# Kernel optimization log

Hardware: AMD Instinct MI355X
Metric: run time of the kernel (lower is better)

## Reference

```python
import jax, jax.numpy as jnp
import numpy as np

B, T, NVAR, H, C = 1024, 96, 7, 64, 3  # batch, seq_len/time-points, nvar, ode_hidden, components
H4 = 4 * H


def setup_inputs() -> dict:
    key = jax.random.key(0)
    ks = jax.random.split(key, 12)
    def w(k, shape, fan_in):
        return (jax.random.normal(k, shape, jnp.float32) / np.sqrt(fan_in)).astype(jnp.float32)
    return {
        "x": jax.random.normal(ks[0], (B, T, NVAR), jnp.float32),
        # init_net: Linear(nvar->H), ReLU, Linear(H->C*H)   (stored as (in,out))
        "init_w1": w(ks[1], (NVAR, H), NVAR), "init_b1": jnp.zeros((H,), jnp.float32),
        "init_w2": w(ks[2], (H, C * H), H),   "init_b2": jnp.zeros((C * H,), jnp.float32),
        # ODEFunc.net: Linear(H+C -> 4H), Tanh, Linear(4H -> H)
        "ode_w1": w(ks[3], (H + C, H4), H + C), "ode_b1": jnp.zeros((H4,), jnp.float32),
        "ode_w2": w(ks[4], (H4, H), H4),        "ode_b2": jnp.zeros((H,), jnp.float32),
        # interaction param (init eye) and frozen conservation linear (eye, no bias)
        "interaction": jnp.eye(C, dtype=jnp.float32),
        "conservation": jnp.eye(C, dtype=jnp.float32),
        # decode_net: per-component Linear(H->H), ReLU, Linear(H->nvar)
        "dec_w1": w(ks[5], (C, H, H), H), "dec_b1": jnp.zeros((C, H), jnp.float32),
        "dec_w2": w(ks[6], (C, H, NVAR), H), "dec_b2": jnp.zeros((C, NVAR), jnp.float32),
        "t_points": jnp.linspace(0.0, 1.0, T).astype(jnp.float32),
    }


def _ode_func(t, state, interaction, conservation, ode_w1, ode_b1, ode_w2, ode_b2):
    # state: (B, C, H)
    b = state.shape[0]
    state_comp = state.mean(axis=-1)                                   # (B, C)
    ie = jnp.einsum('ij,bj->bi', interaction, state_comp)              # bmm(interaction, mean)
    ie = jnp.einsum('oi,bi->bo', conservation, ie)                     # frozen linear (no bias)
    inputs = jnp.concatenate(
        [state.reshape(b * C, H), ie.reshape(b * C, 1), jnp.full((b * C, 1), t, state.dtype)],
        axis=1)                                                        # (B*C, H+2)? no: H + 1 + 1 = H + C since C==3? -> H+2; matches torch cat of [H,1,1] only if C accounts: net expects H+C=H+3.
    # NOTE: torch concatenates [state(H), interaction_effect(1), t(1)] = H+2 features but the
    # Linear expects H+C.  With C=3 torch relies on nn.Linear(H+3) receiving H+2?? It does not --
    # torch code passes H+2 features into Linear(H+C).  Faithful translation pads to match below.
    d = jnp.tanh(inputs @ ode_w1[: inputs.shape[1]] + ode_b1) @ ode_w2 + ode_b2
    return d.reshape(state.shape)


def reference(x, init_w1, init_b1, init_w2, init_b2, ode_w1, ode_b1, ode_w2, ode_b2,
              interaction, conservation, dec_w1, dec_b1, dec_w2, dec_b2, t_points):
    # initial state from mean over sequence
    h0 = jax.nn.relu(x.mean(axis=1) @ init_w1 + init_b1)
    y0 = (h0 @ init_w2 + init_b2).reshape(-1, C, H)                    # (B, C, H)

    f = lambda t, y: _ode_func(t, y, interaction, conservation, ode_w1, ode_b1, ode_w2, ode_b2)

    def rk4_step(y, ts):
        t0, t1 = ts
        h = t1 - t0
        k1 = f(t0, y)
        k2 = f(t0 + 0.5 * h, y + 0.5 * h * k1)
        k3 = f(t0 + 0.5 * h, y + 0.5 * h * k2)
        k4 = f(t1, y + h * k3)
        y1 = y + (h / 6.0) * (k1 + 2.0 * k2 + 2.0 * k3 + k4)
        return y1, y1

    ts = jnp.stack([t_points[:-1], t_points[1:]], axis=1)              # (T-1, 2)
    _, ys = jax.lax.scan(rk4_step, y0, ts)                             # (T-1, B, C, H)
    states = jnp.concatenate([y0[None], ys], axis=0)                   # (T, B, C, H)
    states = jnp.transpose(states, (1, 0, 2, 3))                       # (B, T, C, H)

    # per-component decode MLP
    hid = jax.nn.relu(jnp.einsum('btch,chk->btck', states, dec_w1) + dec_b1)
    comps = jnp.einsum('btck,ckn->btcn', hid, dec_w2) + dec_b2         # (B, T, C, NVAR)
    comps = jnp.moveaxis(comps, 2, 0)                                  # (C, B, T, NVAR)
    # comps[0] is the trend, comps[1:] the high-frequency components
    return comps
```

## Files before the change

kernel.cpp:

```cpp
#include <hip/hip_runtime.h>

#define BTOT 1024
#define TPTS 96
#define NV   7
#define HD   64
#define NH   256

typedef short bf16x8 __attribute__((ext_vector_type(8)));
typedef float f32x4  __attribute__((ext_vector_type(4)));
typedef unsigned int u32x4 __attribute__((ext_vector_type(4)));
#define MFMA16(a,b,c) __builtin_amdgcn_mfma_f32_16x16x32_bf16(a,b,c,0,0,0)

#define OFF_YP   0
#define OFF_TP   1024
#define OFF_PRT  5120
#define OFF_YF   9472
#define OFF_PS   10512
#define OFF_TPS  10576
#define SMEM_WORDS 10672
#define SMEM_BYTES (SMEM_WORDS*4)

__device__ __forceinline__ float rdlane(float v, int i) {
    return __int_as_float(__builtin_amdgcn_readlane(__float_as_int(v), i));
}
__device__ __forceinline__ float wsum64(float v) {
    v += __shfl_xor(v, 1);  v += __shfl_xor(v, 2);  v += __shfl_xor(v, 4);
    v += __shfl_xor(v, 8);  v += __shfl_xor(v, 16); v += __shfl_xor(v, 32);
    return v;
}
__device__ __forceinline__ float tanh_fast(float x) {
    float e = __expf(2.f * x);
    return 1.f - 2.f / (e + 1.f);
}
__device__ __forceinline__ ushort bf16rn(float x) {
    unsigned u = __float_as_uint(x);
    return (ushort)((u + 0x7fffu + ((u >> 16) & 1u)) >> 16);
}
__device__ __forceinline__ void split2(float x, ushort& h, ushort& l) {
    h = bf16rn(x);
    float hf = __uint_as_float(((unsigned)h) << 16);
    l = bf16rn(x - hf);
}

union FU { u32x4 uv; unsigned u[4]; ushort s[8]; bf16x8 v; };

__global__ __launch_bounds__(1024)
void node_mfma6(const float* __restrict__ x,
                const float* __restrict__ iw1, const float* __restrict__ ib1,
                const float* __restrict__ iw2, const float* __restrict__ ib2,
                const float* __restrict__ ow1, const float* __restrict__ ob1,
                const float* __restrict__ ow2, const float* __restrict__ ob2,
                const float* __restrict__ inter, const float* __restrict__ cons,
                const float* __restrict__ dw1, const float* __restrict__ db1,
                const float* __restrict__ dw2, const float* __restrict__ db2,
                const float* __restrict__ tpts,
                float* __restrict__ out)
{
    extern __shared__ float sm[];
    unsigned* YPw = (unsigned*)(sm + OFF_YP);
    unsigned* TPw = (unsigned*)(sm + OFF_TP);
    float*    PRT = sm + OFF_PRT;
    float*    Yf  = sm + OFF_YF;
    float*    PS  = sm + OFF_PS;
    float*    tps = sm + OFF_TPS;

    const int tid = threadIdx.x;
    const int w   = tid >> 6;
    const int ln  = tid & 63;
    const int m   = ln & 15;
    const int g4  = ln >> 4;
    const int nt  = w & 3;
    const int kq  = w >> 2;

    if (tid < TPTS) tps[tid] = tpts[tid];

    const int col1 = 16*w + m;
    FU w1h[2], w1l[2], w2h[2], w2l[2];
    #pragma unroll
    for (int cc = 0; cc < 2; ++cc) {
        #pragma unroll
        for (int j = 0; j < 8; ++j) {
            ushort h, l;
            int k1 = 32*cc + 8*g4 + j;
            split2(ow1[k1*NH + col1], h, l);
            w1h[cc].s[j] = h; w1l[cc].s[j] = l;
            int k2 = 64*kq + 32*cc + 8*g4 + j;
            split2(ow2[k2*HD + 16*nt + m], h, l);
            w2h[cc].s[j] = h; w2l[cc].s[j] = l;
        }
    }
    const float w64c = ow1[64*NH + col1];
    const float w65c = ow1[65*NH + col1];
    const float b1c  = ob1[col1];
    const float b2c  = ob2[16*nt + m];

    const int cpm = m % 3, base3 = m - cpm;
    float Mr0, Mr1, Mr2;
    {
        float I[9], C[9];
        #pragma unroll
        for (int i = 0; i < 9; ++i) { I[i] = inter[i]; C[i] = cons[i]; }
        float M_[3][3];
        #pragma unroll
        for (int r = 0; r < 3; ++r)
            #pragma unroll
            for (int c = 0; c < 3; ++c)
                M_[r][c] = (C[r*3+0]*I[0*3+c] + C[r*3+1]*I[1*3+c] + C[r*3+2]*I[2*3+c]) * (1.f/64.f);
        Mr0 = (cpm==0) ? M_[0][0] : (cpm==1) ? M_[1][0] : M_[2][0];
        Mr1 = (cpm==0) ? M_[0][1] : (cpm==1) ? M_[1][1] : M_[2][1];
        Mr2 = (cpm==0) ? M_[0][2] : (cpm==1) ? M_[1][2] : M_[2][2];
    }

    {
        const int el0 = w >> 2;
        const int b0  = blockIdx.x*4 + el0;
        float xs0,xs1,xs2,xs3,xs4,xs5,xs6;
        {
            const float* xp = x + (size_t)b0 * TPTS * NV + ln * NV;
            float v0=xp[0],v1=xp[1],v2=xp[2],v3=xp[3],v4=xp[4],v5=xp[5],v6=xp[6];
            if (ln < 32) {
                const float* xp2 = xp + 64 * NV;
                v0+=xp2[0]; v1+=xp2[1]; v2+=xp2[2]; v3+=xp2[3]; v4+=xp2[4]; v5+=xp2[5]; v6+=xp2[6];
            }
            xs0=wsum64(v0)*(1.f/96.f); xs1=wsum64(v1)*(1.f/96.f); xs2=wsum64(v2)*(1.f/96.f);
            xs3=wsum64(v3)*(1.f/96.f); xs4=wsum64(v4)*(1.f/96.f); xs5=wsum64(v5)*(1.f/96.f);
            xs6=wsum64(v6)*(1.f/96.f);
        }
        float h0v;
        {
            float a = ib1[ln];
            a = fmaf(xs0, iw1[0*HD+ln], a); a = fmaf(xs1, iw1[1*HD+ln], a);
            a = fmaf(xs2, iw1[2*HD+ln], a); a = fmaf(xs3, iw1[3*HD+ln], a);
            a = fmaf(xs4, iw1[4*HD+ln], a); a = fmaf(xs5, iw1[5*HD+ln], a);
            a = fmaf(xs6, iw1[6*HD+ln], a);
            h0v = fmaxf(a, 0.f);
        }
        float y0a = ib2[ln], y0b = ib2[64+ln], y0c = ib2[128+ln];
        #pragma unroll
        for (int k = 0; k < 64; ++k) {
            float hk = rdlane(h0v, k);
            y0a = fmaf(hk, iw2[k*192 + ln],       y0a);
            y0b = fmaf(hk, iw2[k*192 + 64 + ln],  y0b);
            y0c = fmaf(hk, iw2[k*192 + 128 + ln], y0c);
        }
        if ((w & 3) == 0) {
            float yv[3] = {y0a, y0b, y0c};
            #pragma unroll
            for (int r = 0; r < 3; ++r) {
                int row = el0*3 + r;
                Yf[row*65 + ln] = yv[r];
                ushort hs, ls; split2(yv[r], hs, ls);
                unsigned hp = hs, lp = ls;
                unsigned hq = __shfl_xor(hp, 1), lq = __shfl_xor(lp, 1);
                if ((ln & 1) == 0) {
                    int wgrp = ln >> 3;
                    int woff = row*32 + ((((unsigned)(wgrp ^ row)) & 7) << 2) + ((ln >> 1) & 3);
                    YPw[woff]       = hp | (hq << 16);
                    YPw[512 + woff] = lp | (lq << 16);
                }
            }
            float S0 = wsum64(y0a), S1 = wsum64(y0b), S2 = wsum64(y0c);
            if (ln < 3) PS[el0*3 + ln] = (ln==0)?S0:(ln==1)?S1:S2;
        }
        if (w == 1 && ln >= 12) PS[ln] = 0.f;
        if (w == 2) {
            YPw[384 + ln] = 0u; YPw[448 + ln] = 0u;
            YPw[896 + ln] = 0u; YPw[960 + ln] = 0u;
        }
        if (w == 12) {
            #pragma unroll
            for (int r = 12; r < 16; ++r) Yf[r*65 + ln] = 0.f;
        }
    }
    __syncthreads();

    f32x4 yb, ks;
    if (w < 4) {
        #pragma unroll
        for (int r = 0; r < 4; ++r) yb[r] = Yf[(4*g4 + r)*65 + 16*nt + m];
    }

    auto publish = [&](f32x4 ys, bool commit) {
        #pragma unroll
        for (int r = 0; r < 4; ++r) {
            int row = 4*g4 + r, col = 16*nt + m;
            ushort hs, ls; split2(ys[r], hs, ls);
            unsigned hp = hs, lp = ls;
            unsigned hq = __shfl_xor(hp, 1), lq = __shfl_xor(lp, 1);
            if ((m & 1) == 0) {
                int wgrp = 2*nt + (m >> 3);
                int woff = row*32 + ((((unsigned)(wgrp ^ row)) & 7) << 2) + ((m >> 1) & 3);
                YPw[woff]       = hp | (hq << 16);
                YPw[512 + woff] = lp | (lq << 16);
            }
            if (commit) Yf[row*65 + col] = ys[r];
        }
        float s0 = ys[0], s1 = ys[1], s2 = ys[2], s3 = ys[3];
        #pragma unroll
        for (int d = 1; d < 16; d <<= 1) {
            s0 += __shfl_xor(s0, d); s1 += __shfl_xor(s1, d);
            s2 += __shfl_xor(s2, d); s3 += __shfl_xor(s3, d);
        }
        float sv = (m==0)?s0:(m==1)?s1:(m==2)?s2:s3;
        if (m < 4) PS[nt*16 + 4*g4 + m] = sv;
    };

    auto evalf = [&](float ts, f32x4& dd) {
        float rsum = (PS[m] + PS[16+m]) + (PS[32+m] + PS[48+m]);
        float eAll = Mr0*__shfl(rsum, base3) + Mr1*__shfl(rsum, base3+1) + Mr2*__shfl(rsum, base3+2);

        f32x4 accA = {0,0,0,0}, accB = {0,0,0,0};
        #pragma unroll
        for (int cc = 0; cc < 2; ++cc) {
            FU ah, al;
            int aoff = m*32 + ((((unsigned)((4*cc + g4) ^ m)) & 7) << 2);
            ah.uv = *(const u32x4*)(YPw + aoff);
            al.uv = *(const u32x4*)(YPw + 512 + aoff);
            accA = MFMA16(ah.v, w1h[cc].v, accA);
            accB = MFMA16(ah.v, w1l[cc].v, accB);
            accA = MFMA16(al.v, w1h[cc].v, accA);
        }
        #pragma unroll
        for (int r = 0; r < 4; ++r) {
            float er = __shfl(eAll, 4*g4 + r);
            float val = accA[r] + accB[r];
            val = fmaf(w64c, er, val);
            val = fmaf(w65c, ts, val);
            val += b1c;
            float th = tanh_fast(val);
            ushort hs, ls; split2(th, hs, ls);
            unsigned hp = hs, lp = ls;
            unsigned hq = __shfl_xor(hp, 1), lq = __shfl_xor(lp, 1);
            if ((m & 1) == 0) {
                int row = 4*g4 + r;
                int wgrp = 2*w + (m >> 3);
                int woff = row*128 + (((wgrp & 24) | ((wgrp ^ row) & 7)) << 2) + ((m >> 1) & 3);
                TPw[woff]        = hp | (hq << 16);
                TPw[2048 + woff] = lp | (lq << 16);
            }
        }
        __syncthreads();

        f32x4 pA = {0,0,0,0}, pB = {0,0,0,0};
        #pragma unroll
        for (int cc = 0; cc < 2; ++cc) {
            FU ah, al;
            int aoff = m*128 + 32*kq + ((((unsigned)((4*cc + g4) ^ m)) & 7) << 2);
            ah.uv = *(const u32x4*)(TPw + aoff);
            al.uv = *(const u32x4*)(TPw + 2048 + aoff);
            pA = MFMA16(ah.v, w2h[cc].v, pA);
            pB = MFMA16(ah.v, w2l[cc].v, pB);
            pA = MFMA16(al.v, w2h[cc].v, pA);
        }
        #pragma unroll
        for (int r = 0; r < 4; ++r)
            PRT[w*272 + (4*g4 + r)*17 + m] = pA[r] + pB[r];
        __syncthreads();

        if (w < 4) {
            #pragma unroll
            for (int r = 0; r < 4; ++r) {
                int o = (4*g4 + r)*17 + m;
                dd[r] = b2c + ((PRT[nt*272 + o] + PRT[(nt+4)*272 + o])
                             + (PRT[(nt+8)*272 + o] + PRT[(nt+12)*272 + o]));
            }
        }
    };

    auto decode = [&](int tix) {
        if (w < 12) {
            const int cc = w % 3, el = w / 3;
            const int b  = blockIdx.x*4 + el;
            float acc = db1[cc*HD + ln];
            #pragma unroll 8
            for (int h = 0; h < 64; ++h)
                acc = fmaf(Yf[w*65 + h], dw1[(cc*HD + h)*HD + ln], acc);
            float hid = fmaxf(acc, 0.f);
            const float* w2p = dw2 + (cc*HD + ln)*NV;
            #pragma unroll
            for (int v = 0; v < NV; ++v) {
                float pv = wsum64(hid * w2p[v]);
                if (ln == 0)
                    out[(((size_t)cc*BTOT + b)*TPTS + tix)*NV + v] = pv + db2[cc*NV + v];
            }
        }
    };

    decode(0);
    f32x4 dd;
    #pragma unroll 1
    for (int s = 0; s < TPTS - 1; ++s) {
        const float ta = tps[s], tb = tps[s + 1];
        const float dt = tb - ta, hdt = 0.5f * dt;

        evalf(ta, dd);
        if (w < 4) { ks = dd; publish(yb + hdt*dd, false); }
        __syncthreads();

        evalf(ta + hdt, dd);
        if (w < 4) { ks += 2.f*dd; publish(yb + hdt*dd, false); }
        __syncthreads();

        evalf(ta + hdt, dd);
        if (w < 4) { ks += 2.f*dd; publish(yb + dt*dd, false); }
        __syncthreads();

        evalf(tb, dd);
        if (w < 4) { ks += dd; yb = yb + (dt*(1.f/6.f))*ks; publish(yb, true); }
        __syncthreads();

        decode(s + 1);
    }
}

extern "C" void kernel_launch(void* const* d_in, const int* in_sizes, int n_in,
                              void* d_out, int out_size, void* d_ws, size_t ws_size,
                              hipStream_t stream) {
    const float* x     = (const float*)d_in[0];
    const float* iw1   = (const float*)d_in[1];
    const float* ib1   = (const float*)d_in[2];
    const float* iw2   = (const float*)d_in[3];
    const float* ib2   = (const float*)d_in[4];
    const float* ow1   = (const float*)d_in[5];
    const float* ob1   = (const float*)d_in[6];
    const float* ow2   = (const float*)d_in[7];
    const float* ob2   = (const float*)d_in[8];
    const float* inter = (const float*)d_in[9];
    const float* cons  = (const float*)d_in[10];
    const float* dw1   = (const float*)d_in[11];
    const float* db1   = (const float*)d_in[12];
    const float* dw2   = (const float*)d_in[13];
    const float* db2   = (const float*)d_in[14];
    const float* tpts  = (const float*)d_in[15];
    float* out = (float*)d_out;

    node_mfma6<<<BTOT / 4, 1024, SMEM_BYTES, stream>>>(
        x, iw1, ib1, iw2, ib2, ow1, ob1, ow2, ob2,
        inter, cons, dw1, db1, dw2, db2, tpts, out);
}
```

Measured before the change: 1.318 ms.

## Stage decoder weights in LDS and spread RK4 state update across all waves

Decoder weights and biases are copied once into shared memory, so the per-timestep decode reads them from LDS instead of global memory. The RK4 accumulate and publish step now runs in all 16 waves, each handling one row of the state tile, instead of only 4 waves doing four rows each. The partial-sum reduction buffer is re-laid out so that the stores and loads are 16-byte vector accesses. LDS use grows to about 100 KB per block, and a max dynamic shared memory attribute is set to allow this.

```diff
diff --git a/kernel.cpp b/kernel.cpp
--- a/kernel.cpp
+++ b/kernel.cpp
@@ -14,10 +14,14 @@
 #define OFF_YP   0
 #define OFF_TP   1024
 #define OFF_PRT  5120
-#define OFF_YF   9472
-#define OFF_PS   10512
-#define OFF_TPS  10576
-#define SMEM_WORDS 10672
+#define OFF_YF   10240
+#define OFF_PS   11280
+#define OFF_TPS  11344
+#define OFF_DW1  11440
+#define OFF_DW2  23728
+#define OFF_DB1  25072
+#define OFF_DB2  25264
+#define SMEM_WORDS 25296
 #define SMEM_BYTES (SMEM_WORDS*4)
 
 __device__ __forceinline__ float rdlane(float v, int i) {
@@ -45,7 +49,7 @@
 union FU { u32x4 uv; unsigned u[4]; ushort s[8]; bf16x8 v; };
 
 __global__ __launch_bounds__(1024)
-void node_mfma6(const float* __restrict__ x,
+void node_mfma7(const float* __restrict__ x,
                 const float* __restrict__ iw1, const float* __restrict__ ib1,
                 const float* __restrict__ iw2, const float* __restrict__ ib2,
                 const float* __restrict__ ow1, const float* __restrict__ ob1,
@@ -63,6 +67,10 @@
     float*    Yf  = sm + OFF_YF;
     float*    PS  = sm + OFF_PS;
     float*    tps = sm + OFF_TPS;
+    float*    DW1 = sm + OFF_DW1;
+    float*    DW2 = sm + OFF_DW2;
+    float*    DB1 = sm + OFF_DB1;
+    float*    DB2 = sm + OFF_DB2;
 
     const int tid = threadIdx.x;
     const int w   = tid >> 6;
@@ -72,7 +80,11 @@
     const int nt  = w & 3;
     const int kq  = w >> 2;
 
-    if (tid < TPTS) tps[tid] = tpts[tid];
+    for (int idx = tid; idx < 3*HD*HD; idx += 1024) DW1[idx] = dw1[idx];
+    if (tid < 3*HD)  { for (int v = 0; v < NV; ++v) DW2[tid*NV + v] = dw2[tid*NV + v]; }
+    if (tid < 192)   DB1[tid] = db1[tid];
+    if (tid < 21)    DB2[tid] = db2[tid];
+    if (tid < TPTS)  tps[tid] = tpts[tid];
 
     const int col1 = 16*w + m;
     FU w1h[2], w1l[2], w2h[2], w2l[2];
@@ -175,34 +187,26 @@
     __syncthreads();
 
     f32x4 yb, ks;
-    if (w < 4) {
-        #pragma unroll
-        for (int r = 0; r < 4; ++r) yb[r] = Yf[(4*g4 + r)*65 + 16*nt + m];
-    }
+    #pragma unroll
+    for (int r = 0; r < 4; ++r) yb[r] = Yf[(4*g4 + r)*65 + 16*nt + m];
 
     auto publish = [&](f32x4 ys, bool commit) {
-        #pragma unroll
-        for (int r = 0; r < 4; ++r) {
-            int row = 4*g4 + r, col = 16*nt + m;
-            ushort hs, ls; split2(ys[r], hs, ls);
-            unsigned hp = hs, lp = ls;
-            unsigned hq = __shfl_xor(hp, 1), lq = __shfl_xor(lp, 1);
-            if ((m & 1) == 0) {
-                int wgrp = 2*nt + (m >> 3);
-                int woff = row*32 + ((((unsigned)(wgrp ^ row)) & 7) << 2) + ((m >> 1) & 3);
-                YPw[woff]       = hp | (hq << 16);
-                YPw[512 + woff] = lp | (lq << 16);
-            }
-            if (commit) Yf[row*65 + col] = ys[r];
-        }
-        float s0 = ys[0], s1 = ys[1], s2 = ys[2], s3 = ys[3];
-        #pragma unroll
-        for (int d = 1; d < 16; d <<= 1) {
-            s0 += __shfl_xor(s0, d); s1 += __shfl_xor(s1, d);
-            s2 += __shfl_xor(s2, d); s3 += __shfl_xor(s3, d);
-        }
-        float sv = (m==0)?s0:(m==1)?s1:(m==2)?s2:s3;
-        if (m < 4) PS[nt*16 + 4*g4 + m] = sv;
+        float yv = (kq==0)?ys[0]:(kq==1)?ys[1]:(kq==2)?ys[2]:ys[3];
+        const int row = 4*g4 + kq;
+        ushort hs, ls; split2(yv, hs, ls);
+        unsigned hp = hs, lp = ls;
+        unsigned hq = __shfl_xor(hp, 1), lq = __shfl_xor(lp, 1);
+        if ((m & 1) == 0) {
+            int wgrp = 2*nt + (m >> 3);
+            int woff = row*32 + ((((unsigned)(wgrp ^ row)) & 7) << 2) + ((m >> 1) & 3);
+            YPw[woff]       = hp | (hq << 16);
+            YPw[512 + woff] = lp | (lq << 16);
+        }
+        if (commit) Yf[row*65 + 16*nt + m] = yv;
+        float s = yv;
+        s += __shfl_xor(s, 1); s += __shfl_xor(s, 2);
+        s += __shfl_xor(s, 4); s += __shfl_xor(s, 8);
+        if (m == 0) PS[nt*16 + row] = s;
     };
 
     auto evalf = [&](float ts, f32x4& dd) {
@@ -252,36 +256,34 @@
             pB = MFMA16(ah.v, w2l[cc].v, pB);
             pA = MFMA16(al.v, w2h[cc].v, pA);
         }
-        #pragma unroll
-        for (int r = 0; r < 4; ++r)
-            PRT[w*272 + (4*g4 + r)*17 + m] = pA[r] + pB[r];
-        __syncthreads();
-
-        if (w < 4) {
-            #pragma unroll
-            for (int r = 0; r < 4; ++r) {
-                int o = (4*g4 + r)*17 + m;
-                dd[r] = b2c + ((PRT[nt*272 + o] + PRT[(nt+4)*272 + o])
-                             + (PRT[(nt+8)*272 + o] + PRT[(nt+12)*272 + o]));
-            }
-        }
+        f32x4 pr = pA + pB;
+        *(f32x4*)(PRT + w*320 + m*20 + 4*g4) = pr;
+        __syncthreads();
+
+        const float* pb = PRT + m*20 + 4*g4;
+        f32x4 q0 = *(const f32x4*)(pb + nt*320);
+        f32x4 q1 = *(const f32x4*)(pb + (nt+4)*320);
+        f32x4 q2 = *(const f32x4*)(pb + (nt+8)*320);
+        f32x4 q3 = *(const f32x4*)(pb + (nt+12)*320);
+        f32x4 qq = (q0 + q1) + (q2 + q3);
+        dd[0] = qq[0] + b2c; dd[1] = qq[1] + b2c;
+        dd[2] = qq[2] + b2c; dd[3] = qq[3] + b2c;
     };
 
     auto decode = [&](int tix) {
         if (w < 12) {
             const int cc = w % 3, el = w / 3;
             const int b  = blockIdx.x*4 + el;
-            float acc = db1[cc*HD + ln];
+            float acc = DB1[cc*HD + ln];
             #pragma unroll 8
             for (int h = 0; h < 64; ++h)
-                acc = fmaf(Yf[w*65 + h], dw1[(cc*HD + h)*HD + ln], acc);
+                acc = fmaf(Yf[w*65 + h], DW1[(cc*HD + h)*HD + ln], acc);
             float hid = fmaxf(acc, 0.f);
-            const float* w2p = dw2 + (cc*HD + ln)*NV;
             #pragma unroll
             for (int v = 0; v < NV; ++v) {
-                float pv = wsum64(hid * w2p[v]);
+                float pv = wsum64(hid * DW2[(cc*HD + ln)*NV + v]);
                 if (ln == 0)
-                    out[(((size_t)cc*BTOT + b)*TPTS + tix)*NV + v] = pv + db2[cc*NV + v];
+                    out[(((size_t)cc*BTOT + b)*TPTS + tix)*NV + v] = pv + DB2[cc*NV + v];
             }
         }
     };
@@ -294,19 +296,19 @@
         const float dt = tb - ta, hdt = 0.5f * dt;
 
         evalf(ta, dd);
-        if (w < 4) { ks = dd; publish(yb + hdt*dd, false); }
+        ks = dd; publish(yb + hdt*dd, false);
         __syncthreads();
 
         evalf(ta + hdt, dd);
-        if (w < 4) { ks += 2.f*dd; publish(yb + hdt*dd, false); }
+        ks += 2.f*dd; publish(yb + hdt*dd, false);
         __syncthreads();
 
         evalf(ta + hdt, dd);
-        if (w < 4) { ks += 2.f*dd; publish(yb + dt*dd, false); }
+        ks += 2.f*dd; publish(yb + dt*dd, false);
         __syncthreads();
 
         evalf(tb, dd);
-        if (w < 4) { ks += dd; yb = yb + (dt*(1.f/6.f))*ks; publish(yb, true); }
+        ks += dd; yb = yb + (dt*(1.f/6.f))*ks; publish(yb, true);
         __syncthreads();
 
         decode(s + 1);
@@ -334,7 +336,11 @@
     const float* tpts  = (const float*)d_in[15];
     float* out = (float*)d_out;
 
-    node_mfma6<<<BTOT / 4, 1024, SMEM_BYTES, stream>>>(
+    (void)hipFuncSetAttribute((const void*)node_mfma7,
+                              hipFuncAttributeMaxDynamicSharedMemorySize,
+                              SMEM_BYTES);
+
+    node_mfma7<<<BTOT / 4, 1024, SMEM_BYTES, stream>>>(
         x, iw1, ib1, iw2, ib2, ow1, ob1, ow2, ob2,
         inter, cons, dw1, db1, dw2, db2, tpts, out);
 }
```

Measured after the change: 1.167 ms. 1.13x faster.
